# Optimization experiments

Hardware: AMD Instinct MI355X
Metric: run time of the kernel (lower is better)

The kernel has to match this reference:

```python
import jax, jax.numpy as jnp
import numpy as np

MAX_SCALE_MUL = float(np.log(100.0))
EPS = 1e-12

def _l2norm(t):
    # F.normalize(dim=-1): x / max(||x||_2, eps)
    n = jnp.sqrt(jnp.sum(t * t, axis=-1, keepdims=True))
    return t / jnp.maximum(n, EPS)

def setup_inputs() -> dict:
    key = jax.random.key(0)
    ks = jax.random.split(key, 6)
    B, L, C, H = 2, 2048, 1024, 16
    x = jax.random.normal(ks[0], (B, L, C), dtype=jnp.float32)
    attn_bias = jax.random.normal(ks[1], (1, 1, L, L), dtype=jnp.float32) * 0.02
    W_qkv = jax.random.normal(ks[2], (3 * C, C), dtype=jnp.float32) * (1.0 / np.sqrt(C))
    q_bias = jnp.zeros((C,), dtype=jnp.float32)
    v_bias = jnp.zeros((C,), dtype=jnp.float32)
    scale_mul_1H11 = jnp.full((1, H, 1, 1), np.log(4.0), dtype=jnp.float32)
    W_proj = jax.random.normal(ks[3], (C, C), dtype=jnp.float32) * (1.0 / np.sqrt(C))
    b_proj = jnp.zeros((C,), dtype=jnp.float32)
    return {"x": x, "attn_bias": attn_bias, "W_qkv": W_qkv, "q_bias": q_bias,
            "v_bias": v_bias, "scale_mul_1H11": scale_mul_1H11,
            "W_proj": W_proj, "b_proj": b_proj}

def reference(x, attn_bias, W_qkv, q_bias, v_bias, scale_mul_1H11, W_proj, b_proj):
    B, L, C = x.shape
    H = scale_mul_1H11.shape[1]
    D = C // H
    # qkv projection (no linear bias) + concatenated (q_bias, 0, v_bias)
    bias = jnp.concatenate([q_bias, jnp.zeros_like(q_bias), v_bias])
    pre_qkv = jnp.einsum('blc,oc->blo', x, W_qkv) + bias  # (B,L,3C)
    qkv = pre_qkv.reshape(B, L, 3, H, D).transpose(2, 0, 3, 1, 4)  # (3,B,H,L,D)
    q, k, v = qkv[0], qkv[1], qkv[2]
    # cosine attention: l2-normalize q,k; q scaled by learned per-head scale
    scale_mul = jnp.exp(jnp.minimum(scale_mul_1H11, MAX_SCALE_MUL))
    q = _l2norm(q) * scale_mul
    k = _l2norm(k)
    # slow_attn_original with scale=1 (attn_l2_norm path)
    attn = jnp.einsum('bhld,bhmd->bhlm', q, k) + attn_bias  # (B,H,L,L)
    attn = jax.nn.softmax(attn, axis=-1)
    oup = jnp.einsum('bhlm,bhmd->bhld', attn, v)  # (B,H,L,D)
    oup = oup.transpose(0, 2, 1, 3).reshape(B, L, C)
    return jnp.einsum('blc,oc->blo', oup, W_proj) + b_proj
```

## Files before the change

kernel.cpp:

```cpp
#include <hip/hip_runtime.h>

typedef short bf16x8 __attribute__((ext_vector_type(8)));
typedef short bf16x4 __attribute__((ext_vector_type(4)));
typedef unsigned short u16x8 __attribute__((ext_vector_type(8)));
typedef float f32x4 __attribute__((ext_vector_type(4)));
typedef unsigned int u32x2 __attribute__((ext_vector_type(2)));

#define LOG2E 1.44269504088896340736f

__device__ __forceinline__ float bf2f(unsigned short u) {
  union { unsigned int i; float f; } v; v.i = ((unsigned int)u) << 16; return v.f;
}
__device__ __forceinline__ unsigned short f2bf(float f) {
  union { float fl; unsigned int i; } v; v.fl = f;
  unsigned int r = v.i + 0x7FFFu + ((v.i >> 16) & 1u);
  return (unsigned short)(r >> 16);
}
__device__ __forceinline__ unsigned int cvt_pk_bf16(float lo, float hi) {
  unsigned int d;
  asm("v_cvt_pk_bf16_f32 %0, %1, %2" : "=v"(d) : "v"(lo), "v"(hi));
  return d;
}
__device__ __forceinline__ void gload_lds16(const void* g, void* l) {
  __builtin_amdgcn_global_load_lds(
      (const __attribute__((address_space(1))) void*)g,
      (__attribute__((address_space(3))) void*)l, 16, 0, 0);
}

__global__ __launch_bounds__(256) void cvt_bf16(const float* __restrict__ in,
                                                unsigned short* __restrict__ out, int n8,
                                                float scale) {
  int i = blockIdx.x * 256 + threadIdx.x;
  if (i >= n8) return;
  float4 a = ((const float4*)in)[2 * i];
  float4 b = ((const float4*)in)[2 * i + 1];
  u16x8 o;
  o[0] = f2bf(a.x * scale); o[1] = f2bf(a.y * scale);
  o[2] = f2bf(a.z * scale); o[3] = f2bf(a.w * scale);
  o[4] = f2bf(b.x * scale); o[5] = f2bf(b.y * scale);
  o[6] = f2bf(b.z * scale); o[7] = f2bf(b.w * scale);
  ((u16x8*)out)[i] = o;
}

template <bool F32OUT>
__global__ __launch_bounds__(256) void gemm_nt(const unsigned short* __restrict__ A,
                                               const unsigned short* __restrict__ B,
                                               void* __restrict__ Cout,
                                               const float* __restrict__ bias,
                                               int M, int N, int K) {
  __shared__ __align__(16) unsigned short a_lds[128 * 64];
  __shared__ __align__(16) unsigned short b_lds[128 * 64];
  const int t = threadIdx.x;
  const int lane = t & 63, w = t >> 6;
  const int wm = w >> 1, wn = w & 1;
  const int r16 = lane >> 4, c16 = lane & 15;
  const int m0 = blockIdx.y * 128, n0 = blockIdx.x * 128;
  f32x4 acc[4][4] = {};
  for (int k0 = 0; k0 < K; k0 += 64) {
#pragma unroll
    for (int i = 0; i < 4; ++i) {
      int s = i * 256 + t;
      int row = s >> 3, c = s & 7;
      int cs = c ^ (row & 7);
      gload_lds16(A + (size_t)(m0 + row) * K + k0 + cs * 8, (char*)a_lds + s * 16);
      gload_lds16(B + (size_t)(n0 + row) * K + k0 + cs * 8, (char*)b_lds + s * 16);
    }
    __syncthreads();
#pragma unroll
    for (int ks = 0; ks < 2; ++ks) {
      bf16x8 af[4], bfr[4];
#pragma unroll
      for (int mi = 0; mi < 4; ++mi) {
        int row = wm * 64 + mi * 16 + c16;
        int ch = (r16 + ks * 4) ^ (row & 7);
        af[mi] = *(const bf16x8*)&a_lds[row * 64 + ch * 8];
      }
#pragma unroll
      for (int ni = 0; ni < 4; ++ni) {
        int row = wn * 64 + ni * 16 + c16;
        int ch = (r16 + ks * 4) ^ (row & 7);
        bfr[ni] = *(const bf16x8*)&b_lds[row * 64 + ch * 8];
      }
#pragma unroll
      for (int mi = 0; mi < 4; ++mi)
#pragma unroll
        for (int ni = 0; ni < 4; ++ni)
          acc[mi][ni] = __builtin_amdgcn_mfma_f32_16x16x32_bf16(af[mi], bfr[ni], acc[mi][ni], 0, 0, 0);
    }
    __syncthreads();
  }
#pragma unroll
  for (int mi = 0; mi < 4; ++mi)
#pragma unroll
    for (int ni = 0; ni < 4; ++ni)
#pragma unroll
      for (int r = 0; r < 4; ++r) {
        int m = m0 + wm * 64 + mi * 16 + r16 * 4 + r;
        int n = n0 + wn * 64 + ni * 16 + c16;
        float v = acc[mi][ni][r];
        if constexpr (F32OUT) {
          ((float*)Cout)[(size_t)m * N + n] = v + bias[n];
        } else {
          ((unsigned short*)Cout)[(size_t)m * N + n] = f2bf(v);
        }
      }
}

__global__ __launch_bounds__(256) void norm_pack(const unsigned short* __restrict__ pre,
                                                 const float* __restrict__ q_bias,
                                                 const float* __restrict__ v_bias,
                                                 const float* __restrict__ scale_mul,
                                                 unsigned short* __restrict__ qo,
                                                 unsigned short* __restrict__ ko,
                                                 unsigned short* __restrict__ vto) {
  __shared__ float tl[64][65];
  const int t = threadIdx.x;
  const int li = t >> 2, dq = t & 3;
  const int tile = blockIdx.x;
  const int sl = blockIdx.y;
  const int qkv = sl >> 4, h = sl & 15;
  const int b = tile >> 5, lt = tile & 31;
  const int l = lt * 64 + li;
  const int dbase = dq * 16;
  const unsigned short* src = pre + ((size_t)b * 2048 + l) * 3072 + qkv * 1024 + h * 64 + dbase;
  float v[16];
  bf16x8 x0 = *(const bf16x8*)src;
  bf16x8 x1 = *(const bf16x8*)(src + 8);
#pragma unroll
  for (int j = 0; j < 8; ++j) {
    v[j] = bf2f((unsigned short)x0[j]);
    v[8 + j] = bf2f((unsigned short)x1[j]);
  }
  if (qkv == 0) {
#pragma unroll
    for (int j = 0; j < 16; ++j) v[j] += q_bias[h * 64 + dbase + j];
  } else if (qkv == 2) {
#pragma unroll
    for (int j = 0; j < 16; ++j) v[j] += v_bias[h * 64 + dbase + j];
  }
  if (qkv < 2) {
    float ss = 0.f;
#pragma unroll
    for (int j = 0; j < 16; ++j) ss += v[j] * v[j];
    ss += __shfl_xor(ss, 1);
    ss += __shfl_xor(ss, 2);
    float inv = 1.0f / fmaxf(sqrtf(ss), 1e-12f);
    if (qkv == 0) inv *= __expf(fminf(scale_mul[h], 4.6051701859880914f));
    u16x8 o0, o1;
#pragma unroll
    for (int j = 0; j < 8; ++j) {
      o0[j] = f2bf(v[j] * inv);
      o1[j] = f2bf(v[8 + j] * inv);
    }
    unsigned short* dst = (qkv == 0 ? qo : ko) + ((size_t)(b * 16 + h) * 2048 + l) * 64 + dbase;
    *(u16x8*)dst = o0;
    *(u16x8*)(dst + 8) = o1;
  } else {
#pragma unroll
    for (int j = 0; j < 16; ++j) tl[li][dbase + j] = v[j];
    __syncthreads();
    const int d = li;
    const int lb = dq * 16;
    u16x8 o0, o1;
#pragma unroll
    for (int j = 0; j < 8; ++j) {
      o0[j] = f2bf(tl[lb + j][d]);
      o1[j] = f2bf(tl[lb + 8 + j][d]);
    }
    unsigned short* dst = vto + ((size_t)(b * 16 + h) * 64 + d) * 2048 + lt * 64 + lb;
    *(u16x8*)dst = o0;
    *(u16x8*)(dst + 8) = o1;
  }
}

__global__ __launch_bounds__(256) void attn_fwd(const unsigned short* __restrict__ qb,
                                                const unsigned short* __restrict__ kbuf,
                                                const unsigned short* __restrict__ vtb,
                                                const unsigned short* __restrict__ biasl2,
                                                unsigned short* __restrict__ oup) {
  __shared__ __align__(16) unsigned short k_lds[64 * 64];
  __shared__ __align__(16) unsigned short vt_lds[64 * 64];
  __shared__ __align__(16) unsigned short b_lds[128 * 64];
  __shared__ __align__(16) unsigned short p_lds[128 * 64];
  const int t = threadIdx.x;
  const int lane = t & 63, w = t >> 6;
  const int r16 = lane >> 4, c16 = lane & 15;
  const int bid = blockIdx.x;
  const int swz = (bid & 7) * 64 + (bid >> 3);
  const int bh = swz >> 4;
  const int q0 = (swz & 15) * 128;
  const int h = bh & 15;
  const size_t qk_base = (size_t)bh * 2048 * 64;
  const int srow = t >> 3;
  const int scs = (t & 7) ^ (srow & 7);
  const unsigned short* kp = kbuf + qk_base + (size_t)srow * 64 + scs * 8;
  const unsigned short* vp = vtb + qk_base + (size_t)srow * 2048 + scs * 8;
  const unsigned short* bp = biasl2 + (size_t)(q0 + srow) * 2048 + scs * 8;
  bf16x8 aq[2][2];
#pragma unroll
  for (int qt = 0; qt < 2; ++qt) {
    int row = q0 + w * 32 + qt * 16 + c16;
    const unsigned short* qp = qb + qk_base + (size_t)row * 64 + r16 * 8;
    aq[qt][0] = *(const bf16x8*)qp;
    aq[qt][1] = *(const bf16x8*)(qp + 32);
  }
  f32x4 o[2][4] = {};
  float lsum[2] = {0.f, 0.f};
  const int m7 = c16 & 7;
  const int prow0 = w * 32 + c16;
  const int prow1 = w * 32 + 16 + c16;

  for (int kb0 = 0; kb0 < 2048; kb0 += 64) {
    gload_lds16(kp + (size_t)kb0 * 64, (char*)k_lds + t * 16);
    gload_lds16(kp + (size_t)kb0 * 64 + 32 * 64, (char*)k_lds + t * 16 + 4096);
    gload_lds16(vp + kb0, (char*)vt_lds + t * 16);
    gload_lds16(vp + kb0 + 32 * 2048, (char*)vt_lds + t * 16 + 4096);
#pragma unroll
    for (int i = 0; i < 4; ++i)
      gload_lds16(bp + kb0 + (size_t)i * 32 * 2048, (char*)b_lds + t * 16 + i * 4096);
    __syncthreads();
    f32x4 s4[2][4] = {};
    __builtin_amdgcn_s_setprio(1);
#pragma unroll
    for (int ks = 0; ks < 2; ++ks) {
      bf16x8 bk[4];
#pragma unroll
      for (int mi = 0; mi < 4; ++mi) {
        int row = mi * 16 + c16;
        int ch = (r16 + ks * 4) ^ (row & 7);
        bk[mi] = *(const bf16x8*)&k_lds[row * 64 + ch * 8];
      }
#pragma unroll
      for (int qt = 0; qt < 2; ++qt)
#pragma unroll
        for (int mi = 0; mi < 4; ++mi)
          s4[qt][mi] = __builtin_amdgcn_mfma_f32_16x16x32_bf16(bk[mi], aq[qt][ks], s4[qt][mi], 0, 0, 0);
    }
    __builtin_amdgcn_s_setprio(0);
    float p[2][4][4];
#pragma unroll
    for (int qt = 0; qt < 2; ++qt) {
      const int prow = qt ? prow1 : prow0;
#pragma unroll
      for (int mi = 0; mi < 4; ++mi) {
        int ch = (2 * mi + (r16 >> 1)) ^ m7;
        bf16x4 b4 = *(const bf16x4*)&b_lds[prow * 64 + ch * 8 + 4 * (r16 & 1)];
#pragma unroll
        for (int r = 0; r < 4; ++r)
          p[qt][mi][r] = __builtin_amdgcn_exp2f(
              __builtin_fmaf(s4[qt][mi][r], LOG2E, bf2f((unsigned short)b4[r])));
      }
#pragma unroll
      for (int mi = 0; mi < 4; ++mi)
        lsum[qt] += (p[qt][mi][0] + p[qt][mi][1]) + (p[qt][mi][2] + p[qt][mi][3]);
    }
#pragma unroll
    for (int qt = 0; qt < 2; ++qt) {
      const int prow = qt ? prow1 : prow0;
#pragma unroll
      for (int mi = 0; mi < 4; ++mi) {
        u32x2 pk2;
        pk2[0] = cvt_pk_bf16(p[qt][mi][0], p[qt][mi][1]);
        pk2[1] = cvt_pk_bf16(p[qt][mi][2], p[qt][mi][3]);
        int ch = (2 * mi + (r16 >> 1)) ^ m7;
        ((u32x2*)p_lds)[prow * 16 + ch * 2 + (r16 & 1)] = pk2;
      }
    }
    __builtin_amdgcn_s_setprio(1);
#pragma unroll
    for (int ks = 0; ks < 2; ++ks) {
      bf16x8 ap[2];
#pragma unroll
      for (int qt = 0; qt < 2; ++qt) {
        const int prow = qt ? prow1 : prow0;
        int ch = (4 * ks + r16) ^ m7;
        ap[qt] = *(const bf16x8*)&p_lds[prow * 64 + ch * 8];
      }
#pragma unroll
      for (int nd = 0; nd < 4; ++nd) {
        int drow = nd * 16 + c16;
        int chv = (r16 + ks * 4) ^ (drow & 7);
        bf16x8 bv = *(const bf16x8*)&vt_lds[drow * 64 + chv * 8];
#pragma unroll
        for (int qt = 0; qt < 2; ++qt)
          o[qt][nd] = __builtin_amdgcn_mfma_f32_16x16x32_bf16(ap[qt], bv, o[qt][nd], 0, 0, 0);
      }
    }
    __builtin_amdgcn_s_setprio(0);
    __syncthreads();
  }
  const int b = bh >> 4;
#pragma unroll
  for (int qt = 0; qt < 2; ++qt) {
    float ls = lsum[qt];
    ls += __shfl_xor(ls, 16);
    ls += __shfl_xor(ls, 32);
    const int qrow_g = q0 + w * 32 + qt * 16 + r16 * 4;
#pragma unroll
    for (int r = 0; r < 4; ++r) {
      float lr = __shfl(ls, r16 * 4 + r);
      float inv = 1.0f / lr;
#pragma unroll
      for (int nd = 0; nd < 4; ++nd) {
        int lq = qrow_g + r;
        int d = nd * 16 + c16;
        oup[((size_t)b * 2048 + lq) * 1024 + h * 64 + d] = f2bf(o[qt][nd][r] * inv);
      }
    }
  }
}

extern "C" void kernel_launch(void* const* d_in, const int* in_sizes, int n_in,
                              void* d_out, int out_size, void* d_ws, size_t ws_size,
                              hipStream_t stream) {
  const float* x = (const float*)d_in[0];
  const float* attn_bias = (const float*)d_in[1];
  const float* W_qkv = (const float*)d_in[2];
  const float* q_bias = (const float*)d_in[3];
  const float* v_bias = (const float*)d_in[4];
  const float* scale_mul = (const float*)d_in[5];
  const float* W_proj = (const float*)d_in[6];
  const float* b_proj = (const float*)d_in[7];
  float* out = (float*)d_out;
  char* ws = (char*)d_ws;

  unsigned short* x_bf = (unsigned short*)(ws + 0);
  unsigned short* wqkv_bf = (unsigned short*)(ws + 8388608);
  unsigned short* wproj_bf = (unsigned short*)(ws + 14680064);
  unsigned short* bias_bf = (unsigned short*)(ws + 16777216);
  unsigned short* q_pk = (unsigned short*)(ws + 25165824);
  unsigned short* k_pk = (unsigned short*)(ws + 33554432);
  unsigned short* vt_pk = (unsigned short*)(ws + 41943040);
  unsigned short* oup_bf = (unsigned short*)(ws + 50331648);
  unsigned short* pre_qkv = (unsigned short*)(ws + 58720256);

  cvt_bf16<<<2048, 256, 0, stream>>>(x, x_bf, 524288, 1.0f);
  cvt_bf16<<<1536, 256, 0, stream>>>(W_qkv, wqkv_bf, 393216, 1.0f);
  cvt_bf16<<<512, 256, 0, stream>>>(W_proj, wproj_bf, 131072, 1.0f);
  cvt_bf16<<<2048, 256, 0, stream>>>(attn_bias, bias_bf, 524288, LOG2E);

  gemm_nt<false><<<dim3(24, 32), 256, 0, stream>>>(x_bf, wqkv_bf, (void*)pre_qkv, nullptr,
                                                   4096, 3072, 1024);
  norm_pack<<<dim3(64, 48), 256, 0, stream>>>(pre_qkv, q_bias, v_bias, scale_mul,
                                              q_pk, k_pk, vt_pk);
  attn_fwd<<<512, 256, 0, stream>>>(q_pk, k_pk, vt_pk, bias_bf, oup_bf);
  gemm_nt<true><<<dim3(8, 32), 256, 0, stream>>>(oup_bf, wproj_bf, (void*)out, b_proj,
                                                 4096, 1024, 1024);
}
```

Baseline: 158.1 us.

## Split attention over key halves with combine kernel; merge conversion launches

The attention kernel now splits each query tile's key range into two halves, doubling the grid to 1024 blocks. Each block writes unnormalized fp32 partial outputs and row sums, and a new combine kernel adds the halves, normalizes and converts to bf16. Without a running max, no rescaling is needed for the merge. The bias and P LDS buffers are merged into one to cut shared memory and raise occupancy, and the four conversion launches become a single kernel. The cost is extra fp32 partial traffic, one more launch, and workspace aliasing that reuses the x_bf and pre_qkv regions.

```diff
diff --git a/kernel.cpp b/kernel.cpp
--- a/kernel.cpp
+++ b/kernel.cpp
@@ -27,19 +27,28 @@
       (__attribute__((address_space(3))) void*)l, 16, 0, 0);
 }
 
-__global__ __launch_bounds__(256) void cvt_bf16(const float* __restrict__ in,
-                                                unsigned short* __restrict__ out, int n8,
-                                                float scale) {
+__global__ __launch_bounds__(256) void cvt_all(const float* __restrict__ x,
+                                               const float* __restrict__ wqkv,
+                                               const float* __restrict__ wproj,
+                                               const float* __restrict__ bias,
+                                               unsigned short* __restrict__ xb,
+                                               unsigned short* __restrict__ wqb,
+                                               unsigned short* __restrict__ wpb,
+                                               unsigned short* __restrict__ bb) {
   int i = blockIdx.x * 256 + threadIdx.x;
-  if (i >= n8) return;
-  float4 a = ((const float4*)in)[2 * i];
-  float4 b = ((const float4*)in)[2 * i + 1];
+  const float* src; unsigned short* dst; int off; float scale = 1.0f;
+  if (i < 524288)       { src = x;     dst = xb;  off = i; }
+  else if (i < 917504)  { src = wqkv;  dst = wqb; off = i - 524288; }
+  else if (i < 1048576) { src = wproj; dst = wpb; off = i - 917504; }
+  else                  { src = bias;  dst = bb;  off = i - 1048576; scale = LOG2E; }
+  float4 a = ((const float4*)src)[2 * off];
+  float4 b = ((const float4*)src)[2 * off + 1];
   u16x8 o;
   o[0] = f2bf(a.x * scale); o[1] = f2bf(a.y * scale);
   o[2] = f2bf(a.z * scale); o[3] = f2bf(a.w * scale);
   o[4] = f2bf(b.x * scale); o[5] = f2bf(b.y * scale);
   o[6] = f2bf(b.z * scale); o[7] = f2bf(b.w * scale);
-  ((u16x8*)out)[i] = o;
+  ((u16x8*)dst)[off] = o;
 }
 
 template <bool F32OUT>
@@ -177,20 +186,23 @@
                                                 const unsigned short* __restrict__ kbuf,
                                                 const unsigned short* __restrict__ vtb,
                                                 const unsigned short* __restrict__ biasl2,
-                                                unsigned short* __restrict__ oup) {
+                                                float* __restrict__ op0,
+                                                float* __restrict__ op1,
+                                                float* __restrict__ lsum_part) {
   __shared__ __align__(16) unsigned short k_lds[64 * 64];
   __shared__ __align__(16) unsigned short vt_lds[64 * 64];
-  __shared__ __align__(16) unsigned short b_lds[128 * 64];
-  __shared__ __align__(16) unsigned short p_lds[128 * 64];
+  __shared__ __align__(16) unsigned short bp_lds[128 * 64];
   const int t = threadIdx.x;
   const int lane = t & 63, w = t >> 6;
   const int r16 = lane >> 4, c16 = lane & 15;
   const int bid = blockIdx.x;
-  const int swz = (bid & 7) * 64 + (bid >> 3);
-  const int bh = swz >> 4;
+  const int swz = (bid & 7) * 128 + (bid >> 3);
+  const int bh = swz >> 5;
+  const int split = (swz >> 4) & 1;
   const int q0 = (swz & 15) * 128;
   const int h = bh & 15;
   const size_t qk_base = (size_t)bh * 2048 * 64;
+  const int kbeg = split * 1024;
   const int srow = t >> 3;
   const int scs = (t & 7) ^ (srow & 7);
   const unsigned short* kp = kbuf + qk_base + (size_t)srow * 64 + scs * 8;
@@ -210,14 +222,14 @@
   const int prow0 = w * 32 + c16;
   const int prow1 = w * 32 + 16 + c16;
 
-  for (int kb0 = 0; kb0 < 2048; kb0 += 64) {
+  for (int kb0 = kbeg; kb0 < kbeg + 1024; kb0 += 64) {
     gload_lds16(kp + (size_t)kb0 * 64, (char*)k_lds + t * 16);
     gload_lds16(kp + (size_t)kb0 * 64 + 32 * 64, (char*)k_lds + t * 16 + 4096);
     gload_lds16(vp + kb0, (char*)vt_lds + t * 16);
     gload_lds16(vp + kb0 + 32 * 2048, (char*)vt_lds + t * 16 + 4096);
 #pragma unroll
     for (int i = 0; i < 4; ++i)
-      gload_lds16(bp + kb0 + (size_t)i * 32 * 2048, (char*)b_lds + t * 16 + i * 4096);
+      gload_lds16(bp + kb0 + (size_t)i * 32 * 2048, (char*)bp_lds + t * 16 + i * 4096);
     __syncthreads();
     f32x4 s4[2][4] = {};
     __builtin_amdgcn_s_setprio(1);
@@ -244,7 +256,7 @@
 #pragma unroll
       for (int mi = 0; mi < 4; ++mi) {
         int ch = (2 * mi + (r16 >> 1)) ^ m7;
-        bf16x4 b4 = *(const bf16x4*)&b_lds[prow * 64 + ch * 8 + 4 * (r16 & 1)];
+        bf16x4 b4 = *(const bf16x4*)&bp_lds[prow * 64 + ch * 8 + 4 * (r16 & 1)];
 #pragma unroll
         for (int r = 0; r < 4; ++r)
           p[qt][mi][r] = __builtin_amdgcn_exp2f(
@@ -263,7 +275,7 @@
         pk2[0] = cvt_pk_bf16(p[qt][mi][0], p[qt][mi][1]);
         pk2[1] = cvt_pk_bf16(p[qt][mi][2], p[qt][mi][3]);
         int ch = (2 * mi + (r16 >> 1)) ^ m7;
-        ((u32x2*)p_lds)[prow * 16 + ch * 2 + (r16 & 1)] = pk2;
+        ((u32x2*)bp_lds)[prow * 16 + ch * 2 + (r16 & 1)] = pk2;
       }
     }
     __builtin_amdgcn_s_setprio(1);
@@ -274,7 +286,7 @@
       for (int qt = 0; qt < 2; ++qt) {
         const int prow = qt ? prow1 : prow0;
         int ch = (4 * ks + r16) ^ m7;
-        ap[qt] = *(const bf16x8*)&p_lds[prow * 64 + ch * 8];
+        ap[qt] = *(const bf16x8*)&bp_lds[prow * 64 + ch * 8];
       }
 #pragma unroll
       for (int nd = 0; nd < 4; ++nd) {
@@ -289,25 +301,44 @@
     __builtin_amdgcn_s_setprio(0);
     __syncthreads();
   }
-  const int b = bh >> 4;
+  float* op = split ? op1 : op0;
 #pragma unroll
   for (int qt = 0; qt < 2; ++qt) {
     float ls = lsum[qt];
     ls += __shfl_xor(ls, 16);
     ls += __shfl_xor(ls, 32);
+    if (r16 == 0)
+      lsum_part[(size_t)split * 65536 + (size_t)bh * 2048 + q0 + w * 32 + qt * 16 + c16] = ls;
     const int qrow_g = q0 + w * 32 + qt * 16 + r16 * 4;
 #pragma unroll
-    for (int r = 0; r < 4; ++r) {
-      float lr = __shfl(ls, r16 * 4 + r);
-      float inv = 1.0f / lr;
-#pragma unroll
-      for (int nd = 0; nd < 4; ++nd) {
-        int lq = qrow_g + r;
-        int d = nd * 16 + c16;
-        oup[((size_t)b * 2048 + lq) * 1024 + h * 64 + d] = f2bf(o[qt][nd][r] * inv);
-      }
-    }
-  }
+    for (int r = 0; r < 4; ++r)
+#pragma unroll
+      for (int nd = 0; nd < 4; ++nd)
+        op[((size_t)bh * 2048 + qrow_g + r) * 64 + nd * 16 + c16] = o[qt][nd][r];
+  }
+}
+
+__global__ __launch_bounds__(256) void combine(const float* __restrict__ op0,
+                                               const float* __restrict__ op1,
+                                               const float* __restrict__ lsum_part,
+                                               unsigned short* __restrict__ oup) {
+  int gid = blockIdx.x * 256 + threadIdx.x;
+  int d0 = (gid & 7) * 8;
+  int bhl = gid >> 3;
+  int l = bhl & 2047, bh = bhl >> 11;
+  int b = bh >> 4, h = bh & 15;
+  size_t obase = ((size_t)bh * 2048 + l) * 64 + d0;
+  float4 a0 = ((const float4*)(op0 + obase))[0];
+  float4 a1 = ((const float4*)(op0 + obase))[1];
+  float4 c0 = ((const float4*)(op1 + obase))[0];
+  float4 c1 = ((const float4*)(op1 + obase))[1];
+  float inv = 1.0f / (lsum_part[(size_t)bh * 2048 + l] + lsum_part[65536 + (size_t)bh * 2048 + l]);
+  u16x8 o;
+  o[0] = f2bf((a0.x + c0.x) * inv); o[1] = f2bf((a0.y + c0.y) * inv);
+  o[2] = f2bf((a0.z + c0.z) * inv); o[3] = f2bf((a0.w + c0.w) * inv);
+  o[4] = f2bf((a1.x + c1.x) * inv); o[5] = f2bf((a1.y + c1.y) * inv);
+  o[6] = f2bf((a1.z + c1.z) * inv); o[7] = f2bf((a1.w + c1.w) * inv);
+  *(u16x8*)(oup + ((size_t)b * 2048 + l) * 1024 + h * 64 + d0) = o;
 }
 
 extern "C" void kernel_launch(void* const* d_in, const int* in_sizes, int n_in,
@@ -326,24 +357,26 @@
 
   unsigned short* x_bf = (unsigned short*)(ws + 0);
   unsigned short* wqkv_bf = (unsigned short*)(ws + 8388608);
-  unsigned short* wproj_bf = (unsigned short*)(ws + 14680064);
   unsigned short* bias_bf = (unsigned short*)(ws + 16777216);
   unsigned short* q_pk = (unsigned short*)(ws + 25165824);
   unsigned short* k_pk = (unsigned short*)(ws + 33554432);
   unsigned short* vt_pk = (unsigned short*)(ws + 41943040);
   unsigned short* oup_bf = (unsigned short*)(ws + 50331648);
   unsigned short* pre_qkv = (unsigned short*)(ws + 58720256);
-
-  cvt_bf16<<<2048, 256, 0, stream>>>(x, x_bf, 524288, 1.0f);
-  cvt_bf16<<<1536, 256, 0, stream>>>(W_qkv, wqkv_bf, 393216, 1.0f);
-  cvt_bf16<<<512, 256, 0, stream>>>(W_proj, wproj_bf, 131072, 1.0f);
-  cvt_bf16<<<2048, 256, 0, stream>>>(attn_bias, bias_bf, 524288, LOG2E);
-
+  float* o_part0 = (float*)(ws + 58720256);
+  float* o_part1 = (float*)(ws + 0);
+  unsigned short* wproj_bf = (unsigned short*)(ws + 83886080);
+  float* lsum_part = (float*)(ws + 85983232);
+
+  cvt_all<<<6144, 256, 0, stream>>>(x, W_qkv, W_proj, attn_bias,
+                                    x_bf, wqkv_bf, wproj_bf, bias_bf);
   gemm_nt<false><<<dim3(24, 32), 256, 0, stream>>>(x_bf, wqkv_bf, (void*)pre_qkv, nullptr,
                                                    4096, 3072, 1024);
   norm_pack<<<dim3(64, 48), 256, 0, stream>>>(pre_qkv, q_bias, v_bias, scale_mul,
                                               q_pk, k_pk, vt_pk);
-  attn_fwd<<<512, 256, 0, stream>>>(q_pk, k_pk, vt_pk, bias_bf, oup_bf);
+  attn_fwd<<<1024, 256, 0, stream>>>(q_pk, k_pk, vt_pk, bias_bf,
+                                     o_part0, o_part1, lsum_part);
+  combine<<<2048, 256, 0, stream>>>(o_part0, o_part1, lsum_part, oup_bf);
   gemm_nt<true><<<dim3(8, 32), 256, 0, stream>>>(oup_bf, wproj_bf, (void*)out, b_proj,
                                                  4096, 1024, 1024);
 }
```

After: 169.2 us. 7.0% more time.
